# Performance work log

Hardware: AMD Instinct MI355X
Metric: run time of the kernel (lower is better)

The kernel has to match this reference:

```python
import jax, jax.numpy as jnp
import numpy as np

NEG_INF = -1e9  # matches masked_fill value in torch code
LRELU_ALPHA = 0.2


def setup_inputs() -> dict:
    key = jax.random.key(0)
    k1, k2, k3, k4 = jax.random.split(key, 4)
    B, N, F_IN, H, DK = 4, 2048, 128, 4, 32
    x = jax.random.normal(k1, (B, N, F_IN), dtype=jnp.float32)
    adj = jax.random.randint(k2, (B, N, N), 0, 2, dtype=jnp.int32)
    # xavier-ish scaled params
    W = jax.random.normal(k3, (H, F_IN, DK), dtype=jnp.float32) * (1.0 / np.sqrt(F_IN))
    a = jax.random.normal(k4, (H, 2 * DK, 1), dtype=jnp.float32) * (1.0 / np.sqrt(2 * DK))
    return {"x": x, "adj": adj, "W": W, "a": a}


def reference(x, adj, W, a):
    B, N, _ = x.shape
    H, _, DK = W.shape
    # h: (B, H, N, DK)
    h = jnp.einsum('bni,hio->bhno', x, W)
    # Split attention vector: e[b,h,i,j] = h_i.a_l + h_j.a_r  (avoids O(N^2 * 2d) concat)
    a_l = a[:, :DK, 0]   # (H, DK)
    a_r = a[:, DK:, 0]   # (H, DK)
    el = jnp.einsum('bhnd,hd->bhn', h, a_l)  # (B, H, N)
    er = jnp.einsum('bhnd,hd->bhn', h, a_r)  # (B, H, N)
    e = el[:, :, :, None] + er[:, :, None, :]          # (B, H, N, N)
    e = jax.nn.leaky_relu(e, negative_slope=LRELU_ALPHA)
    e = jnp.where(adj[:, None, :, :] == 0, NEG_INF, e)
    alpha = jax.nn.softmax(e, axis=-1)                 # dropout is identity (eval)
    h_prime = jnp.einsum('bhij,bhjd->bhid', alpha, h)  # (B, H, N, DK)
    # torch code does h_prime.view(B, N, -1) on contiguous (B,H,N,DK): raw reshape
    out = h_prime.reshape(B, N, H * DK)
    return out
```

## Files before the change

### kernel.cpp

```cpp
#include <hip/hip_runtime.h>
#include <stdint.h>

#define LOG2E 1.4426950408889634f

typedef __bf16 v8bf __attribute__((ext_vector_type(8)));
typedef float v4f __attribute__((ext_vector_type(4)));
typedef float v16f __attribute__((ext_vector_type(16)));

static constexpr int B = 4, N = 2048, FIN = 128, H = 4, DK = 32;
static constexpr int IT = N / 32;

__device__ __forceinline__ float exp2_fast(float x) {
#if __has_builtin(__builtin_amdgcn_exp2f)
  return __builtin_amdgcn_exp2f(x);
#else
  float r;
  asm("v_exp_f32 %0, %1" : "=v"(r) : "v"(x));
  return r;
#endif
}

__device__ __forceinline__ unsigned int bf16_rne(float f) {
  unsigned int u = __builtin_bit_cast(unsigned int, f);
  u += 0x7FFFu + ((u >> 16) & 1u);
  return u >> 16;
}

__device__ __forceinline__ v8bf pack8(const float* v) {
  uint4 u;
  u.x = bf16_rne(v[0]) | (bf16_rne(v[1]) << 16);
  u.y = bf16_rne(v[2]) | (bf16_rne(v[3]) << 16);
  u.z = bf16_rne(v[4]) | (bf16_rne(v[5]) << 16);
  u.w = bf16_rne(v[6]) | (bf16_rne(v[7]) << 16);
  return __builtin_bit_cast(v8bf, u);
}

__global__ __launch_bounds__(256) void k_hproj(const float* __restrict__ x,
                                               const float* __restrict__ W,
                                               const float* __restrict__ a,
                                               unsigned short* __restrict__ h_t,
                                               float* __restrict__ el,
                                               float* __restrict__ er) {
  int blk = blockIdx.x;
  int b = blk >> 6, it = blk & 63;
  int tid = threadIdx.x;
  int head = tid >> 6, lane = tid & 63;
  int lrow = lane & 31, kh = lane >> 5;
  int bh = b * H + head;
  int n = it * 32 + lrow;
  const float* xp = x + (b * N + n) * FIN + kh * 8;
  const float* wp = W + head * FIN * DK + lrow;
  v16f acc = {};
#pragma unroll
  for (int s = 0; s < FIN / 16; ++s) {
    float xv[8], wv[8];
    *(float4*)&xv[0] = *(const float4*)(xp + s * 16);
    *(float4*)&xv[4] = *(const float4*)(xp + s * 16 + 4);
    int fb = s * 16 + kh * 8;
#pragma unroll
    for (int k = 0; k < 8; ++k) wv[k] = wp[(fb + k) * DK];
    acc = __builtin_amdgcn_mfma_f32_32x32x16_bf16(pack8(wv), pack8(xv), acc, 0, 0, 0);
  }
  float pel = 0.f, per = 0.f;
#pragma unroll
  for (int r = 0; r < 16; ++r) {
    int d = (r & 3) + 8 * (r >> 2) + 4 * kh;
    float hv = acc[r];
    h_t[(bh * DK + d) * N + n] = (unsigned short)bf16_rne(hv);
    pel = fmaf(hv, a[head * 2 * DK + d], pel);
    per = fmaf(hv, a[head * 2 * DK + DK + d], per);
  }
  pel += __shfl_xor(pel, 32);
  per += __shfl_xor(per, 32);
  if (kh == 0) {
    el[bh * N + n] = pel * LOG2E;
    er[bh * N + n] = per * LOG2E;
  }
}

__global__ __launch_bounds__(1024, 6) void k_attn(const int* __restrict__ adj,
                                                  const unsigned short* __restrict__ h_t,
                                                  const float* __restrict__ el,
                                                  const float* __restrict__ er,
                                                  float* __restrict__ out) {
  __shared__ float ersh[H * N];
  __shared__ float part[H * 16 * DK];
  __shared__ float lsh[H * 16];
  int blk = blockIdx.x;
  int b = blk >> 7, it16 = blk & 127;
  int tid = threadIdx.x;
  int wave = tid >> 6;
  int head = wave & 3, jq = wave >> 2;
  int lane = tid & 63;
  int m = lane & 15, kg = lane >> 4;
  int bh = b * H + head;
  int ig = it16 * 16 + m;

  {
    int hh = tid >> 8, t = tid & 255;
    const float4* es = (const float4*)(er + (b * H + hh) * N);
    float4* ed = (float4*)ersh;
    ed[hh * 512 + t] = es[t];
    ed[hh * 512 + 256 + t] = es[256 + t];
  }
  part[tid] = 0.f;
  part[tid + 1024] = 0.f;
  if (tid < H * 16) lsh[tid] = 0.f;
  __syncthreads();

  float eli = el[bh * N + ig];
  int j0 = jq * 512 + kg * 8;
  const int* arow = adj + (size_t)(b * N + ig) * N + j0;
  const unsigned short* hp0 = h_t + (size_t)(bh * DK + m) * N + j0;
  const unsigned short* hp1 = hp0 + 16 * N;
  const float* ep = ersh + head * N + j0;

  v4f acc0 = {}, acc1 = {};
  float lsum = 0.f;

  int4 Aa = *(const int4*)(arow);
  int4 Ab = *(const int4*)(arow + 4);
  int4 Hb0 = *(const int4*)(hp0);
  int4 Hb1 = *(const int4*)(hp1);

  for (int s = 0; s < 16; ++s) {
    int4 aa = Aa, ab = Ab, h0 = Hb0, h1 = Hb1;
    if (s + 1 < 16) {
      int o = (s + 1) * 32;
      Aa = *(const int4*)(arow + o);
      Ab = *(const int4*)(arow + o + 4);
      Hb0 = *(const int4*)(hp0 + o);
      Hb1 = *(const int4*)(hp1 + o);
    }
    float4 ea = *(const float4*)(ep + s * 32);
    float4 eb = *(const float4*)(ep + s * 32 + 4);
    int ad[8] = {aa.x, aa.y, aa.z, aa.w, ab.x, ab.y, ab.z, ab.w};
    float ev[8] = {ea.x, ea.y, ea.z, ea.w, eb.x, eb.y, eb.z, eb.w};
    unsigned ub[8];
#pragma unroll
    for (int k = 0; k < 8; ++k) {
      float tt = eli + ev[k];
      tt = fmaxf(tt, 0.2f * tt);
      float pv = exp2_fast(tt);
      unsigned u = __builtin_bit_cast(unsigned, pv) & 0xFFFF0000u;
      u = ad[k] ? u : 0u;
      ub[k] = u;
      lsum += __builtin_bit_cast(float, u);
    }
    unsigned u0 = __builtin_amdgcn_perm(ub[1], ub[0], 0x07060302u);
    unsigned u1 = __builtin_amdgcn_perm(ub[3], ub[2], 0x07060302u);
    unsigned u2 = __builtin_amdgcn_perm(ub[5], ub[4], 0x07060302u);
    unsigned u3 = __builtin_amdgcn_perm(ub[7], ub[6], 0x07060302u);
    uint4 au = {u0, u1, u2, u3};
    v8bf av = __builtin_bit_cast(v8bf, au);
    acc0 = __builtin_amdgcn_mfma_f32_16x16x32_bf16(av, __builtin_bit_cast(v8bf, h0),
                                                   acc0, 0, 0, 0);
    acc1 = __builtin_amdgcn_mfma_f32_16x16x32_bf16(av, __builtin_bit_cast(v8bf, h1),
                                                   acc1, 0, 0, 0);
  }

  lsum += __shfl_xor(lsum, 16);
  lsum += __shfl_xor(lsum, 32);
  if (lane < 16) atomicAdd(&lsh[head * 16 + lane], lsum);
#pragma unroll
  for (int r = 0; r < 4; ++r) {
    int row = kg * 4 + r;
    atomicAdd(&part[(head * 16 + row) * DK + m], acc0[r]);
    atomicAdd(&part[(head * 16 + row) * DK + 16 + m], acc1[r]);
  }
  __syncthreads();

  if (tid < 512) {
    int gd = tid * 4;
    int rh = gd >> 9, ri = (gd >> 5) & 15, rd = gd & 31;
    float inv = 1.0f / lsh[rh * 16 + ri];
    float4 s4 = *(const float4*)&part[(rh * 16 + ri) * DK + rd];
    float4 o = {s4.x * inv, s4.y * inv, s4.z * inv, s4.w * inv};
    *(float4*)&out[(size_t)((b * H + rh) * N + it16 * 16 + ri) * DK + rd] = o;
  }
}

extern "C" void kernel_launch(void* const* d_in, const int* in_sizes, int n_in,
                              void* d_out, int out_size, void* d_ws, size_t ws_size,
                              hipStream_t stream) {
  const float* x = (const float*)d_in[0];
  const int* adj = (const int*)d_in[1];
  const float* W = (const float*)d_in[2];
  const float* a = (const float*)d_in[3];
  float* out = (float*)d_out;
  char* ws = (char*)d_ws;

  unsigned short* h_t = (unsigned short*)(ws);
  float* el = (float*)(ws + 0x200000);
  float* er = (float*)(ws + 0x220000);

  hipLaunchKernelGGL(k_hproj, dim3(B * IT), dim3(256), 0, stream, x, W, a, h_t, el, er);
  hipLaunchKernelGGL(k_attn, dim3(B * (N / 16)), dim3(1024), 0, stream, adj, h_t, el, er, out);
}
```

Before: 157.6 us.

## Pre-pack adjacency into bitmasks and compute softmax denominator via MFMA

Adds a separate kernel that ballots the int32 adjacency matrix into 1-bit masks. The attention kernel then loads each block's 16 rows of mask into LDS instead of streaming the int32 adjacency per element. The row sum of the unnormalized weights is now computed by an extra MFMA against a ones column, replacing the scalar accumulation and shuffles. Reading the full int32 adjacency still happens once in the pack kernel, so total traffic falls only modestly, and the change adds a kernel launch, an intermediate buffer, and an extra MFMA per step.

```diff
diff --git a/kernel.cpp b/kernel.cpp
--- a/kernel.cpp
+++ b/kernel.cpp
@@ -33,6 +33,24 @@
   u.z = bf16_rne(v[4]) | (bf16_rne(v[5]) << 16);
   u.w = bf16_rne(v[6]) | (bf16_rne(v[7]) << 16);
   return __builtin_bit_cast(v8bf, u);
+}
+
+__global__ __launch_bounds__(256) void k_pack(const int* __restrict__ adj,
+                                              unsigned int* __restrict__ adjb) {
+  int wid = (blockIdx.x * 256 + threadIdx.x) >> 6;
+  int lane = threadIdx.x & 63;
+  const int* p = adj + (size_t)wid * 256 + lane;
+  unsigned long long m0 = __ballot(p[0] != 0);
+  unsigned long long m1 = __ballot(p[64] != 0);
+  unsigned long long m2 = __ballot(p[128] != 0);
+  unsigned long long m3 = __ballot(p[192] != 0);
+  if (lane == 0) {
+    uint4 v0 = {(unsigned)m0, (unsigned)(m0 >> 32), (unsigned)m1, (unsigned)(m1 >> 32)};
+    uint4 v1 = {(unsigned)m2, (unsigned)(m2 >> 32), (unsigned)m3, (unsigned)(m3 >> 32)};
+    uint4* dst = (uint4*)(adjb + (size_t)wid * 8);
+    dst[0] = v0;
+    dst[1] = v1;
+  }
 }
 
 __global__ __launch_bounds__(256) void k_hproj(const float* __restrict__ x,
@@ -78,14 +96,15 @@
   }
 }
 
-__global__ __launch_bounds__(1024, 6) void k_attn(const int* __restrict__ adj,
-                                                  const unsigned short* __restrict__ h_t,
-                                                  const float* __restrict__ el,
-                                                  const float* __restrict__ er,
-                                                  float* __restrict__ out) {
+__global__ __launch_bounds__(1024) void k_attn(const unsigned int* __restrict__ adjb,
+                                               const unsigned short* __restrict__ h_t,
+                                               const float* __restrict__ el,
+                                               const float* __restrict__ er,
+                                               float* __restrict__ out) {
   __shared__ float ersh[H * N];
   __shared__ float part[H * 16 * DK];
   __shared__ float lsh[H * 16];
+  __shared__ unsigned amask[16 * 65];
   int blk = blockIdx.x;
   int b = blk >> 7, it16 = blk & 127;
   int tid = threadIdx.x;
@@ -103,6 +122,10 @@
     ed[hh * 512 + t] = es[t];
     ed[hh * 512 + 256 + t] = es[256 + t];
   }
+  {
+    int row = tid >> 6, dw = tid & 63;
+    amask[row * 65 + dw] = adjb[(size_t)(b * N + it16 * 16 + row) * 64 + dw];
+  }
   part[tid] = 0.f;
   part[tid + 1024] = 0.f;
   if (tid < H * 16) lsh[tid] = 0.f;
@@ -110,31 +133,30 @@
 
   float eli = el[bh * N + ig];
   int j0 = jq * 512 + kg * 8;
-  const int* arow = adj + (size_t)(b * N + ig) * N + j0;
   const unsigned short* hp0 = h_t + (size_t)(bh * DK + m) * N + j0;
   const unsigned short* hp1 = hp0 + 16 * N;
   const float* ep = ersh + head * N + j0;
-
-  v4f acc0 = {}, acc1 = {};
-  float lsum = 0.f;
-
-  int4 Aa = *(const int4*)(arow);
-  int4 Ab = *(const int4*)(arow + 4);
+  int shbase = kg * 8;
+
+  unsigned oc = (m == 0) ? 0x3F803F80u : 0u;
+  uint4 ou = {oc, oc, oc, oc};
+  v8bf ones_f = __builtin_bit_cast(v8bf, ou);
+
+  v4f acc0 = {}, acc1 = {}, acc2 = {};
+
   int4 Hb0 = *(const int4*)(hp0);
   int4 Hb1 = *(const int4*)(hp1);
 
   for (int s = 0; s < 16; ++s) {
-    int4 aa = Aa, ab = Ab, h0 = Hb0, h1 = Hb1;
+    int4 h0 = Hb0, h1 = Hb1;
     if (s + 1 < 16) {
       int o = (s + 1) * 32;
-      Aa = *(const int4*)(arow + o);
-      Ab = *(const int4*)(arow + o + 4);
       Hb0 = *(const int4*)(hp0 + o);
       Hb1 = *(const int4*)(hp1 + o);
     }
+    unsigned mdw = amask[m * 65 + jq * 16 + s];
     float4 ea = *(const float4*)(ep + s * 32);
     float4 eb = *(const float4*)(ep + s * 32 + 4);
-    int ad[8] = {aa.x, aa.y, aa.z, aa.w, ab.x, ab.y, ab.z, ab.w};
     float ev[8] = {ea.x, ea.y, ea.z, ea.w, eb.x, eb.y, eb.z, eb.w};
     unsigned ub[8];
 #pragma unroll
@@ -142,10 +164,8 @@
       float tt = eli + ev[k];
       tt = fmaxf(tt, 0.2f * tt);
       float pv = exp2_fast(tt);
-      unsigned u = __builtin_bit_cast(unsigned, pv) & 0xFFFF0000u;
-      u = ad[k] ? u : 0u;
-      ub[k] = u;
-      lsum += __builtin_bit_cast(float, u);
+      unsigned bit = (mdw >> (shbase + k)) & 1u;
+      ub[k] = __builtin_bit_cast(unsigned, pv) & (0u - bit);
     }
     unsigned u0 = __builtin_amdgcn_perm(ub[1], ub[0], 0x07060302u);
     unsigned u1 = __builtin_amdgcn_perm(ub[3], ub[2], 0x07060302u);
@@ -157,16 +177,18 @@
                                                    acc0, 0, 0, 0);
     acc1 = __builtin_amdgcn_mfma_f32_16x16x32_bf16(av, __builtin_bit_cast(v8bf, h1),
                                                    acc1, 0, 0, 0);
-  }
-
-  lsum += __shfl_xor(lsum, 16);
-  lsum += __shfl_xor(lsum, 32);
-  if (lane < 16) atomicAdd(&lsh[head * 16 + lane], lsum);
+    acc2 = __builtin_amdgcn_mfma_f32_16x16x32_bf16(av, ones_f, acc2, 0, 0, 0);
+  }
+
 #pragma unroll
   for (int r = 0; r < 4; ++r) {
     int row = kg * 4 + r;
     atomicAdd(&part[(head * 16 + row) * DK + m], acc0[r]);
     atomicAdd(&part[(head * 16 + row) * DK + 16 + m], acc1[r]);
+  }
+  if (m == 0) {
+#pragma unroll
+    for (int r = 0; r < 4; ++r) atomicAdd(&lsh[head * 16 + kg * 4 + r], acc2[r]);
   }
   __syncthreads();
 
@@ -193,7 +215,9 @@
   unsigned short* h_t = (unsigned short*)(ws);
   float* el = (float*)(ws + 0x200000);
   float* er = (float*)(ws + 0x220000);
-
+  unsigned int* adjb = (unsigned int*)(ws + 0x240000);
+
+  hipLaunchKernelGGL(k_pack, dim3(B * N * N / 1024), dim3(256), 0, stream, adj, adjb);
   hipLaunchKernelGGL(k_hproj, dim3(B * IT), dim3(256), 0, stream, x, W, a, h_t, el, er);
-  hipLaunchKernelGGL(k_attn, dim3(B * (N / 16)), dim3(1024), 0, stream, adj, h_t, el, er, out);
-}
+  hipLaunchKernelGGL(k_attn, dim3(B * (N / 16)), dim3(1024), 0, stream, adjb, h_t, el, er, out);
+}
```

New measurement: 152.5 us. -3.2%, faster.
